# Performance work log

Measured on AMD Instinct MI355X. Metric: run time of the kernel, lower is better.

The kernel has to match this reference:

```python
import jax, jax.numpy as jnp
import numpy as np

B, H, L, D = 2, 16, 1024, 64
LMAX = 2048  # max_sequence_length: patterns built & normalized at LMAX, then sliced to L
PI = float(np.pi)


def _scale_pattern(freq):
    # pattern[h, t, d] = exp(i(t+ph)) + exp(i(2t+ph)) + exp(i(0.5t+ph)), ph = 2*pi*h/H
    # identical across d, so keep [H, L, 1] and broadcast over D
    phase = 2.0 * PI * jnp.arange(H, dtype=jnp.float32) / H          # [H]
    t = jnp.linspace(0.0, 2.0 * PI * freq, LMAX)                     # [LMAX]
    a1 = t[None, :] + phase[:, None]
    a2 = 2.0 * t[None, :] + phase[:, None]
    a3 = 0.5 * t[None, :] + phase[:, None]
    pr = jnp.cos(a1) + jnp.cos(a2) + jnp.cos(a3)                     # [H, LMAX]
    pi_ = jnp.sin(a1) + jnp.sin(a2) + jnp.sin(a3)
    norm = jnp.sqrt(jnp.sum(pr * pr + pi_ * pi_, axis=1, keepdims=True))  # over full LMAX
    pr, pi_ = pr / norm, pi_ / norm
    return pr[:, :L, None], pi_[:, :L, None]                          # [H, L, 1]


def _expert_total_pattern():
    # 8 experts x 3 aspects; pattern[t, d] = exp(i(f*t + 2*pi*d/D)), normalized per
    # column over LMAX (|exp|=1 -> norm sqrt(LMAX)). Elementwise complex multiply is
    # linear, so the expert stage equals x * sum(all patterns)/(sqrt(3)*sqrt(8)).
    freqs = np.array([[0.3 + 0.1 * i, 0.2 + 0.1 * i, 0.1 + 0.1 * i]
                      for i in range(8)], dtype=np.float32).reshape(-1)   # [24]
    t = jnp.linspace(0.0, 2.0 * PI, LMAX)                                 # [LMAX]
    phase_d = 2.0 * PI * jnp.arange(D, dtype=jnp.float32) / D             # [D]
    ang = jnp.asarray(freqs)[:, None, None] * t[None, :, None] + phase_d[None, None, :]  # [24, LMAX, D]
    col_norm = 1.0 / np.sqrt(float(LMAX))
    denom = np.sqrt(3.0) * np.sqrt(8.0)
    pr = jnp.sum(jnp.cos(ang), axis=0) * (col_norm / denom)               # [LMAX, D]
    pi_ = jnp.sum(jnp.sin(ang), axis=0) * (col_norm / denom)
    return pr[:L], pi_[:L]                                                # [L, D]


def _process_scale(Qr, Qi, Kr, Ki, Vr, Vi, pr, pi_):
    # complex elementwise pattern multiply
    Qpr = Qr * pr - Qi * pi_
    Qpi = Qr * pi_ + Qi * pr
    Kpr = Kr * pr - Ki * pi_
    Kpi = Kr * pi_ + Ki * pr
    # complex scores = Qp @ Kp^T (no conjugation, matching the torch code)
    sr = jnp.einsum('bhld,bhmd->bhlm', Qpr, Kpr) - jnp.einsum('bhld,bhmd->bhlm', Qpi, Kpi)
    si = jnp.einsum('bhld,bhmd->bhlm', Qpr, Kpi) + jnp.einsum('bhld,bhmd->bhlm', Qpi, Kpr)
    mag = jnp.sqrt(sr * sr + si * si) / np.sqrt(float(D))
    w = jax.nn.softmax(mag, axis=-1)
    return (jnp.einsum('bhlm,bhmd->bhld', w, Vr),
            jnp.einsum('bhlm,bhmd->bhld', w, Vi))


def reference(Q_real, Q_imag, K_real, K_imag, V_real, V_imag):
    scale_freqs = [1.0, 0.5, 0.25, 0.1]  # char, word, phrase, sentence
    acc_r = jnp.zeros_like(Q_real)
    acc_i = jnp.zeros_like(Q_real)
    for f in scale_freqs:
        pr, pi_ = _scale_pattern(f)
        o_r, o_i = _process_scale(Q_real, Q_imag, K_real, K_imag, V_real, V_imag, pr, pi_)
        acc_r = acc_r + o_r
        acc_i = acc_i + o_i
    inv = 1.0 / np.sqrt(float(len(scale_freqs)))
    acc_r = acc_r * inv
    acc_i = acc_i * inv
    # expert mixing (linear in x -> single fused complex elementwise multiply)
    epr, epi = _expert_total_pattern()  # [L, D], broadcast over B,H
    out_r = acc_r * epr - acc_i * epi
    out_i = acc_r * epi + acc_i * epr
    return jnp.stack([out_r, out_i], axis=0)  # [2, B, H, L, D] (real, imag)


def setup_inputs() -> dict:
    key = jax.random.key(0)
    ks = jax.random.split(key, 6)
    shape = (B, H, L, D)
    names = ['Q_real', 'Q_imag', 'K_real', 'K_imag', 'V_real', 'V_imag']
    return {n: jax.random.normal(k, shape, dtype=jnp.float32) for n, k in zip(names, ks)}
```

## Files before the change

### kernel.cpp

```cpp
#include <hip/hip_runtime.h>
#include <math.h>

typedef short bf16x8 __attribute__((ext_vector_type(8)));
typedef float f32x4 __attribute__((ext_vector_type(4)));

#define BDIM 256
#define ADIM 512
constexpr int B_ = 2, H_ = 16, L_ = 1024, D_ = 64, LMAX_ = 2048;
constexpr int BH_ = B_ * H_;
constexpr float PI_F = 3.14159265358979323846f;

constexpr int WS_SVP = 0;
constexpr int WS_KBR = 65536;
constexpr int WS_KBI = WS_KBR + 1048576;
constexpr int WS_VTR = WS_KBI + 1048576;
constexpr int WS_VTI = WS_VTR + 1048576;

__device__ __forceinline__ unsigned short f2b(float x) {
    union { float f; unsigned u; } v; v.f = x;
    return (unsigned short)((v.u + 0x8000u) >> 16);
}
__device__ __forceinline__ float b2f(unsigned short x) {
    union { unsigned u; float f; } v; v.u = ((unsigned)x) << 16;
    return v.f;
}
__device__ __forceinline__ unsigned pk2(float a, float b) {
    union { float f; unsigned u; } va, vb; va.f = a; vb.f = b;
    return ((va.u + 0x8000u) >> 16) | ((vb.u + 0x8000u) & 0xFFFF0000u);
}
__device__ __forceinline__ uint4 pack4(const float4& a, const float4& b) {
    return make_uint4(pk2(a.x, a.y), pk2(a.z, a.w), pk2(b.x, b.y), pk2(b.z, b.w));
}
__device__ __forceinline__ unsigned cvtpk(float lo, float hi) {
    unsigned r;
    asm("v_cvt_pk_bf16_f32 %0, %1, %2" : "=v"(r) : "v"(lo), "v"(hi));
    return r;
}
__device__ __forceinline__ float vsqrt(float x) {
    float r;
    asm("v_sqrt_f32 %0, %1" : "=v"(r) : "v"(x));
    return r;
}

#define MFMA(a, b, c) __builtin_amdgcn_mfma_f32_16x16x32_bf16((a), (b), (c), 0, 0, 0)

__device__ __forceinline__ float a_val(int s, int l, float4 invn) {
    const float fr = (s == 0) ? 1.0f : (s == 1) ? 0.5f : (s == 2) ? 0.25f : 0.1f;
    const float iv = (s == 0) ? invn.x : (s == 1) ? invn.y : (s == 2) ? invn.z : invn.w;
    float t = (2.0f * PI_F * fr / (float)(LMAX_ - 1)) * (float)l;
    float m2 = 3.0f + 2.0f * cosf(t) + 2.0f * cosf(0.5f * t) + 2.0f * cosf(1.5f * t);
    return sqrtf(fmaxf(m2, 0.0f)) * iv;
}

__global__ __launch_bounds__(BDIM)
void prep_kernel(const float* __restrict__ Kr, const float* __restrict__ Ki,
                 const float* __restrict__ Vr, const float* __restrict__ Vi,
                 float* __restrict__ ws) {
    const int tid = threadIdx.x;
    const int blk = blockIdx.x;
    unsigned short* KbR = (unsigned short*)(ws + WS_KBR);
    unsigned short* KbI = (unsigned short*)(ws + WS_KBI);
    unsigned short* VtR = (unsigned short*)(ws + WS_VTR);
    unsigned short* VtI = (unsigned short*)(ws + WS_VTI);

    if (blk < 256) {
        const int comp = blk >> 7;
        const float* src = comp ? Ki : Kr;
        unsigned short* dst = comp ? KbI : KbR;
        size_t b0 = (size_t)(blk & 127) * 16384;
#pragma unroll
        for (int i = 0; i < 4; ++i) {
            size_t e = b0 + (size_t)(i * 256 + tid) * 16;
            float4 x0 = *(const float4*)(src + e);
            float4 x1 = *(const float4*)(src + e + 4);
            float4 x2 = *(const float4*)(src + e + 8);
            float4 x3 = *(const float4*)(src + e + 12);
            *(uint4*)(dst + e) = pack4(x0, x1);
            *(uint4*)(dst + e + 8) = pack4(x2, x3);
        }
    } else {
        __shared__ unsigned short sT[64 * 70];
        __shared__ float sRed[4 * 64];
        const int vb = blk - 256;
        const int comp = vb & 1, mt = (vb >> 1) & 15, bh = vb >> 5;
        const int m0 = mt * 64;
        const float* src = (comp ? Vi : Vr) + (size_t)bh * 65536 + (size_t)m0 * 64;
        unsigned short* dstA = (comp ? VtI : VtR) + (size_t)bh * 65536;
#pragma unroll
        for (int i = 0; i < 4; ++i) {
            int e = i * 256 + tid;
            int m = e >> 4, d4 = (e & 15) * 4;
            float4 x = *(const float4*)(src + (size_t)m * 64 + d4);
            *(uint2*)&sT[m * 70 + d4] = make_uint2(pk2(x.x, x.y), pk2(x.z, x.w));
        }
        {
            int d = tid & 63, grp = tid >> 6;
            float s = 0.0f;
#pragma unroll
            for (int k = 0; k < 16; ++k) s += src[(size_t)(grp * 16 + k) * 64 + d];
            sRed[grp * 64 + d] = s;
        }
        __syncthreads();
        {
            int d = tid >> 2, ms = (tid & 3) * 16;
            unsigned short v[16];
#pragma unroll
            for (int k = 0; k < 16; ++k) v[k] = sT[(ms + k) * 70 + d];
            unsigned short* dst = dstA + (size_t)d * 1024 + m0 + ms;
            *(uint4*)dst = make_uint4((unsigned)v[0] | ((unsigned)v[1] << 16),
                                      (unsigned)v[2] | ((unsigned)v[3] << 16),
                                      (unsigned)v[4] | ((unsigned)v[5] << 16),
                                      (unsigned)v[6] | ((unsigned)v[7] << 16));
            *(uint4*)(dst + 8) = make_uint4((unsigned)v[8] | ((unsigned)v[9] << 16),
                                            (unsigned)v[10] | ((unsigned)v[11] << 16),
                                            (unsigned)v[12] | ((unsigned)v[13] << 16),
                                            (unsigned)v[14] | ((unsigned)v[15] << 16));
        }
        if (tid < 64)
            ws[WS_SVP + comp * 32768 + bh * 1024 + tid * 16 + mt] =
                sRed[tid] + sRed[64 + tid] + sRed[128 + tid] + sRed[192 + tid];
    }
}

__device__ __forceinline__ void stage64s(const unsigned short* g0, int stride,
                                         unsigned short* lds, int w, int lane) {
#pragma unroll
    for (int i = 0; i < 2; ++i) {
        int c = w * 2 + i;
        int lrow = c * 8 + (lane >> 3);
        int lg = (lane & 7) ^ (lrow & 7);
        const unsigned short* src = g0 + (size_t)lrow * stride + lg * 8;
        __builtin_amdgcn_global_load_lds(
            (const __attribute__((address_space(1))) void*)src,
            (__attribute__((address_space(3))) void*)(lds + c * 512), 16, 0, 0);
    }
}
__device__ __forceinline__ bf16x8 ldfrag(const unsigned short* b, int row, int g) {
    return *(const bf16x8*)&b[row * 64 + ((g ^ (row & 7)) << 3)];
}

constexpr int OFF_DEN = 0;
constexpr int OFF_K0  = 2048;
constexpr int OFF_K1  = OFF_K0 + 16384;
constexpr int OFF_V0  = OFF_K1 + 16384;
constexpr int OFF_V1  = OFF_V0 + 16384;
constexpr int OFF_E   = OFF_V1 + 16384;
constexpr int OFF_MG  = OFF_E + 16384;
constexpr int OFF_AMB = OFF_MG + 16384;
constexpr int SMEM_BYTES = OFF_AMB + 8256;

__global__ __launch_bounds__(ADIM, 2)
void attn_kernel_w(const float* __restrict__ Qr, const float* __restrict__ Qi,
                   const float* __restrict__ ws, float* __restrict__ out, float4 invn) {
    extern __shared__ char smem[];
    float* sDen = (float*)(smem + OFF_DEN);
    unsigned short* sK0 = (unsigned short*)(smem + OFF_K0);
    unsigned short* sK1 = (unsigned short*)(smem + OFF_K1);
    unsigned short* sV0 = (unsigned short*)(smem + OFF_V0);
    unsigned short* sV1 = (unsigned short*)(smem + OFF_V1);
    unsigned short* sE  = (unsigned short*)(smem + OFF_E);
    unsigned short* sMg = (unsigned short*)(smem + OFF_MG);
    unsigned short* sAmb = (unsigned short*)(smem + OFF_AMB);

    const int tid = threadIdx.x;
    const int lane = tid & 63;
    const int w = tid >> 6;
    const int lo16 = lane & 15;
    const int quad = lane >> 4;
    const int blk = blockIdx.x;
    const int bh = (blk & 7) * 4 + (blk >> 6);
    const int qt = (blk >> 3) & 7;
    const int l0 = qt * 128;
    const size_t base = (size_t)bh * (L_ * D_);

    const unsigned short* gKr = (const unsigned short*)(ws + WS_KBR) + (size_t)bh * 65536;
    const unsigned short* gKi = (const unsigned short*)(ws + WS_KBI) + (size_t)bh * 65536;
    const unsigned short* gVr = (const unsigned short*)(ws + WS_VTR) + (size_t)bh * 65536;
    const unsigned short* gVi = (const unsigned short*)(ws + WS_VTI) + (size_t)bh * 65536;

    if (w < 4) {
        stage64s(gKr, 64, sK0, w, lane);
        stage64s(gKi, 64, sK1, w, lane);
    } else {
        stage64s(gVr, 1024, sV0, w - 4, lane);
        stage64s(gVi, 1024, sV1, w - 4, lane);
    }

    for (int e = tid; e < 4096; e += ADIM) {
        int s = e >> 10, l = e & 1023;
        sAmb[s * 1032 + l] = f2b(a_val(s, l, invn) * 0.125f);
    }

    bf16x8 fQr0, fQr1, fQi0, fQi1, fnQi0, fnQi1;
    {
        const int ql = l0 + w * 16 + lo16;
        const float* qr = Qr + base + (size_t)ql * 64;
        const float* qi = Qi + base + (size_t)ql * 64;
        float4 a0 = *(const float4*)(qr + quad * 8);
        float4 a1 = *(const float4*)(qr + quad * 8 + 4);
        float4 b0 = *(const float4*)(qr + 32 + quad * 8);
        float4 b1 = *(const float4*)(qr + 32 + quad * 8 + 4);
        *(uint4*)&fQr0 = pack4(a0, a1);
        *(uint4*)&fQr1 = pack4(b0, b1);
        a0 = *(const float4*)(qi + quad * 8);
        a1 = *(const float4*)(qi + quad * 8 + 4);
        b0 = *(const float4*)(qi + 32 + quad * 8);
        b1 = *(const float4*)(qi + 32 + quad * 8 + 4);
        *(uint4*)&fQi0 = pack4(a0, a1);
        *(uint4*)&fQi1 = pack4(b0, b1);
        uint4 t0 = *(uint4*)&fQi0, t1 = *(uint4*)&fQi1;
        t0.x ^= 0x80008000u; t0.y ^= 0x80008000u; t0.z ^= 0x80008000u; t0.w ^= 0x80008000u;
        t1.x ^= 0x80008000u; t1.y ^= 0x80008000u; t1.z ^= 0x80008000u; t1.w ^= 0x80008000u;
        *(uint4*)&fnQi0 = t0; *(uint4*)&fnQi1 = t1;
    }

    __syncthreads();

    bf16x8 uf1a = (bf16x8){0, 0, 0, 0, 0, 0, 0, 0};
    uf1a[0] = (short)f2b(b2f(sAmb[quad * 1032 + (l0 + w * 16 + lo16)]) *
                         (1.0f / 128.0f));

    f32x4 accM1 = (f32x4){0.f, 0.f, 0.f, 0.f};
    f32x4 aOutR[4], aOutI[4];
#pragma unroll
    for (int dt = 0; dt < 4; ++dt) {
        aOutR[dt] = (f32x4){0.f, 0.f, 0.f, 0.f};
        aOutI[dt] = (f32x4){0.f, 0.f, 0.f, 0.f};
    }

#pragma unroll 1
    for (int mt = 0; mt < 16; ++mt) {
        const int m0 = mt * 64;
        const int cur = mt & 1;
        if (mt < 15) {
            if (w < 4) {
                stage64s(gKr + (size_t)(m0 + 64) * 64, 64, sK0 + (cur ^ 1) * 4096, w, lane);
                stage64s(gKi + (size_t)(m0 + 64) * 64, 64, sK1 + (cur ^ 1) * 4096, w, lane);
            } else {
                stage64s(gVr + m0 + 64, 1024, sV0 + (cur ^ 1) * 4096, w - 4, lane);
                stage64s(gVi + m0 + 64, 1024, sV1 + (cur ^ 1) * 4096, w - 4, lane);
            }
        }
        const unsigned short* cK0 = sK0 + cur * 4096;
        const unsigned short* cK1 = sK1 + cur * 4096;
        const unsigned short* cV0 = sV0 + cur * 4096;
        const unsigned short* cV1 = sV1 + cur * 4096;

#pragma unroll
        for (int ct = 0; ct < 4; ++ct) {
            const int mrow = ct * 16 + lo16;
            bf16x8 kr0 = ldfrag(cK0, mrow, quad), kr1 = ldfrag(cK0, mrow, quad + 4);
            bf16x8 ki0 = ldfrag(cK1, mrow, quad), ki1 = ldfrag(cK1, mrow, quad + 4);
            f32x4 aR = (f32x4){0.f, 0.f, 0.f, 0.f};
            f32x4 aI = (f32x4){0.f, 0.f, 0.f, 0.f};
            __builtin_amdgcn_s_setprio(1);
            aR = MFMA(kr0, fQr0, aR);  aR = MFMA(kr1, fQr1, aR);
            aR = MFMA(ki0, fnQi0, aR); aR = MFMA(ki1, fnQi1, aR);
            aI = MFMA(ki0, fQr0, aI);  aI = MFMA(ki1, fQr1, aI);
            aI = MFMA(kr0, fQi0, aI);  aI = MFMA(kr1, fQi1, aI);
            __builtin_amdgcn_s_setprio(0);
            float mg0 = vsqrt(fmaf(aR[0], aR[0], aI[0] * aI[0]));
            float mg1 = vsqrt(fmaf(aR[1], aR[1], aI[1] * aI[1]));
            float mg2 = vsqrt(fmaf(aR[2], aR[2], aI[2] * aI[2]));
            float mg3 = vsqrt(fmaf(aR[3], aR[3], aI[3] * aI[3]));
            bf16x8 bf1 = (bf16x8){0, 0, 0, 0, 0, 0, 0, 0};
            bf1[0] = (short)sAmb[quad * 1032 + m0 + ct * 16 + lo16];
            f32x4 z = (f32x4){0.f, 0.f, 0.f, 0.f};
            f32x4 a1 = MFMA(bf1, uf1a, z);
            float p0 = mg0 * a1[0], p1 = mg1 * a1[1];
            float p2 = mg2 * a1[2], p3 = mg3 * a1[3];
            int l = w * 16 + lo16;
            int gph = (ct * 2 + (quad >> 1)) ^ (l & 7);
            *(uint2*)&sE[l * 64 + gph * 8 + (quad & 1) * 4] =
                make_uint2(cvtpk(p0, p1), cvtpk(p2, p3));
            *(uint2*)&sMg[l * 64 + gph * 8 + (quad & 1) * 4] =
                make_uint2(cvtpk(mg0, mg1), cvtpk(mg2, mg3));
        }
        {
            bf16x8 mf0 = ldfrag(sMg, w * 16 + lo16, quad);
            bf16x8 mf1 = ldfrag(sMg, w * 16 + lo16, quad + 4);
            bf16x8 b0 = (bf16x8){0, 0, 0, 0, 0, 0, 0, 0};
            bf16x8 b1 = (bf16x8){0, 0, 0, 0, 0, 0, 0, 0};
            if (lo16 < 4) {
                b0 = *(const bf16x8*)&sAmb[lo16 * 1032 + m0 + quad * 8];
                b1 = *(const bf16x8*)&sAmb[lo16 * 1032 + m0 + 32 + quad * 8];
            }
            accM1 = MFMA(mf0, b0, accM1);
            accM1 = MFMA(mf1, b1, accM1);
        }
        {
            bf16x8 pa0 = ldfrag(sE, w * 16 + lo16, quad);
            bf16x8 pa1 = ldfrag(sE, w * 16 + lo16, quad + 4);
            __builtin_amdgcn_s_setprio(1);
#pragma unroll
            for (int dt = 0; dt < 4; ++dt) {
                int dr = dt * 16 + lo16;
                bf16x8 vr0 = ldfrag(cV0, dr, quad), vr1 = ldfrag(cV0, dr, quad + 4);
                bf16x8 vi0 = ldfrag(cV1, dr, quad), vi1 = ldfrag(cV1, dr, quad + 4);
                aOutR[dt] = MFMA(pa0, vr0, aOutR[dt]);
                aOutR[dt] = MFMA(pa1, vr1, aOutR[dt]);
                aOutI[dt] = MFMA(pa0, vi0, aOutI[dt]);
                aOutI[dt] = MFMA(pa1, vi1, aOutI[dt]);
            }
            __builtin_amdgcn_s_setprio(0);
        }
        asm volatile("s_waitcnt vmcnt(0)" ::: "memory");
        __builtin_amdgcn_s_barrier();
    }

    if (lo16 < 4) {
#pragma unroll
        for (int reg = 0; reg < 4; ++reg) {
            int r = w * 16 + quad * 4 + reg;
            float alv = b2f(sAmb[lo16 * 1032 + (l0 + r)]) * 8.0f;
            sDen[lo16 * 128 + r] = 1.0f / (1024.0f + alv * accM1[reg]);
        }
    }
    float cden[4];
#pragma unroll
    for (int reg = 0; reg < 4; ++reg) {
        int r = w * 16 + quad * 4 + reg;
        cden[reg] = sDen[r] + sDen[128 + r] + sDen[256 + r] + sDen[384 + r];
    }

    const float cE = rsqrtf(2048.0f) * rsqrtf(24.0f);
    float eRr[4], eRi[4];
#pragma unroll
    for (int reg = 0; reg < 4; ++reg) {
        int lrow = l0 + w * 16 + quad * 4 + reg;
        float tl = (2.0f * PI_F / (float)(LMAX_ - 1)) * (float)lrow;
        float s1, c1;
        __sincosf(0.1f * tl, &s1, &c1);
        const float W[10] = {1.f, 2.f, 3.f, 3.f, 3.f, 3.f, 3.f, 3.f, 2.f, 1.f};
        float cr = c1, ci = s1;
        float er = W[0] * cr, ei = W[0] * ci;
#pragma unroll
        for (int k = 1; k < 10; ++k) {
            float nr = cr * c1 - ci * s1;
            float ni = cr * s1 + ci * c1;
            cr = nr; ci = ni;
            er = fmaf(W[k], cr, er);
            ei = fmaf(W[k], ci, ei);
        }
        eRr[reg] = er * cE;
        eRi[reg] = ei * cE;
    }

    const size_t ooff = (size_t)BH_ * L_ * D_;
#pragma unroll
    for (int dt = 0; dt < 4; ++dt) {
        int d = dt * 16 + lo16;
        const float* svp = ws + WS_SVP + bh * 1024 + (size_t)d * 16;
        float4 r0 = *(const float4*)(svp);
        float4 r1 = *(const float4*)(svp + 4);
        float4 r2 = *(const float4*)(svp + 8);
        float4 r3 = *(const float4*)(svp + 12);
        float svr = (r0.x + r0.y + r0.z + r0.w) + (r1.x + r1.y + r1.z + r1.w) +
                    (r2.x + r2.y + r2.z + r2.w) + (r3.x + r3.y + r3.z + r3.w);
        const float* svq = svp + 32768;
        r0 = *(const float4*)(svq);
        r1 = *(const float4*)(svq + 4);
        r2 = *(const float4*)(svq + 8);
        r3 = *(const float4*)(svq + 12);
        float svi = (r0.x + r0.y + r0.z + r0.w) + (r1.x + r1.y + r1.z + r1.w) +
                    (r2.x + r2.y + r2.z + r2.w) + (r3.x + r3.y + r3.z + r3.w);
        float sp, cp;
        __sincosf((2.0f * PI_F / 64.0f) * (float)d, &sp, &cp);
#pragma unroll
        for (int reg = 0; reg < 4; ++reg) {
            int lrow = l0 + w * 16 + quad * 4 + reg;
            float numR = fmaf(cden[reg], svr, aOutR[dt][reg]) * 0.5f;
            float numI = fmaf(cden[reg], svi, aOutI[dt][reg]) * 0.5f;
            float epr = cp * eRr[reg] - sp * eRi[reg];
            float epi = sp * eRr[reg] + cp * eRi[reg];
            size_t o = base + (size_t)lrow * 64 + d;
            out[o] = numR * epr - numI * epi;
            out[o + ooff] = numR * epi + numI * epr;
        }
    }
}

__global__ __launch_bounds__(BDIM, 2)
void attn_kernel(const float* __restrict__ Qr, const float* __restrict__ Qi,
                 const float* __restrict__ ws, float* __restrict__ out, float4 invn) {
    __shared__ unsigned short sK0[2][4096], sK1[2][4096];
    __shared__ unsigned short sV0[4096], sV1[4096];
    __shared__ unsigned short sE[4096];
    __shared__ unsigned short sMg[4096];
    __shared__ unsigned short sAmb[4 * 1032];
    __shared__ float sDen[4 * 64];

    const int tid = threadIdx.x;
    const int lane = tid & 63;
    const int w = tid >> 6;
    const int lo16 = lane & 15;
    const int quad = lane >> 4;
    const int blk = blockIdx.x;
    const int bh = (blk & 7) * 4 + (blk >> 7);
    const int qt = (blk >> 3) & 15;
    const int l0 = qt * 64;
    const size_t base = (size_t)bh * (L_ * D_);

    const unsigned short* gKr = (const unsigned short*)(ws + WS_KBR) + (size_t)bh * 65536;
    const unsigned short* gKi = (const unsigned short*)(ws + WS_KBI) + (size_t)bh * 65536;
    const unsigned short* gVr = (const unsigned short*)(ws + WS_VTR) + (size_t)bh * 65536;
    const unsigned short* gVi = (const unsigned short*)(ws + WS_VTI) + (size_t)bh * 65536;

    stage64s(gKr, 64, sK0[0], w, lane);
    stage64s(gKi, 64, sK1[0], w, lane);

    for (int e = tid; e < 4096; e += BDIM) {
        int s = e >> 10, l = e & 1023;
        sAmb[s * 1032 + l] = f2b(a_val(s, l, invn) * 0.125f);
    }

    bf16x8 fQr0, fQr1, fQi0, fQi1, fnQi0, fnQi1;
    {
        const int ql = l0 + w * 16 + lo16;
        const float* qr = Qr + base + (size_t)ql * 64;
        const float* qi = Qi + base + (size_t)ql * 64;
        float4 a0 = *(const float4*)(qr + quad * 8);
        float4 a1 = *(const float4*)(qr + quad * 8 + 4);
        float4 b0 = *(const float4*)(qr + 32 + quad * 8);
        float4 b1 = *(const float4*)(qr + 32 + quad * 8 + 4);
        *(uint4*)&fQr0 = pack4(a0, a1);
        *(uint4*)&fQr1 = pack4(b0, b1);
        a0 = *(const float4*)(qi + quad * 8);
        a1 = *(const float4*)(qi + quad * 8 + 4);
        b0 = *(const float4*)(qi + 32 + quad * 8);
        b1 = *(const float4*)(qi + 32 + quad * 8 + 4);
        *(uint4*)&fQi0 = pack4(a0, a1);
        *(uint4*)&fQi1 = pack4(b0, b1);
        uint4 t0 = *(uint4*)&fQi0, t1 = *(uint4*)&fQi1;
        t0.x ^= 0x80008000u; t0.y ^= 0x80008000u; t0.z ^= 0x80008000u; t0.w ^= 0x80008000u;
        t1.x ^= 0x80008000u; t1.y ^= 0x80008000u; t1.z ^= 0x80008000u; t1.w ^= 0x80008000u;
        *(uint4*)&fnQi0 = t0; *(uint4*)&fnQi1 = t1;
    }

    __syncthreads();

    bf16x8 uf1a = (bf16x8){0, 0, 0, 0, 0, 0, 0, 0};
    uf1a[0] = (short)f2b(b2f(sAmb[quad * 1032 + (l0 + w * 16 + lo16)]) *
                         (1.0f / 128.0f));

    f32x4 accM1 = (f32x4){0.f, 0.f, 0.f, 0.f};
    f32x4 aOutR[4], aOutI[4];
#pragma unroll
    for (int dt = 0; dt < 4; ++dt) {
        aOutR[dt] = (f32x4){0.f, 0.f, 0.f, 0.f};
        aOutI[dt] = (f32x4){0.f, 0.f, 0.f, 0.f};
    }

#pragma unroll 1
    for (int mt = 0; mt < 16; ++mt) {
        const int m0 = mt * 64;
        const int cur = mt & 1;
        stage64s(gVr + m0, 1024, sV0, w, lane);
        stage64s(gVi + m0, 1024, sV1, w, lane);
        if (mt < 15) {
            stage64s(gKr + (size_t)(m0 + 64) * 64, 64, sK0[cur ^ 1], w, lane);
            stage64s(gKi + (size_t)(m0 + 64) * 64, 64, sK1[cur ^ 1], w, lane);
        }
        const unsigned short* cK0 = sK0[cur];
        const unsigned short* cK1 = sK1[cur];

#pragma unroll
        for (int ct = 0; ct < 4; ++ct) {
            const int mrow = ct * 16 + lo16;
            bf16x8 kr0 = ldfrag(cK0, mrow, quad), kr1 = ldfrag(cK0, mrow, quad + 4);
            bf16x8 ki0 = ldfrag(cK1, mrow, quad), ki1 = ldfrag(cK1, mrow, quad + 4);
            f32x4 aR = (f32x4){0.f, 0.f, 0.f, 0.f};
            f32x4 aI = (f32x4){0.f, 0.f, 0.f, 0.f};
            __builtin_amdgcn_s_setprio(1);
            aR = MFMA(kr0, fQr0, aR);  aR = MFMA(kr1, fQr1, aR);
            aR = MFMA(ki0, fnQi0, aR); aR = MFMA(ki1, fnQi1, aR);
            aI = MFMA(ki0, fQr0, aI);  aI = MFMA(ki1, fQr1, aI);
            aI = MFMA(kr0, fQi0, aI);  aI = MFMA(kr1, fQi1, aI);
            __builtin_amdgcn_s_setprio(0);
            float mg0 = vsqrt(fmaf(aR[0], aR[0], aI[0] * aI[0]));
            float mg1 = vsqrt(fmaf(aR[1], aR[1], aI[1] * aI[1]));
            float mg2 = vsqrt(fmaf(aR[2], aR[2], aI[2] * aI[2]));
            float mg3 = vsqrt(fmaf(aR[3], aR[3], aI[3] * aI[3]));
            bf16x8 bf1 = (bf16x8){0, 0, 0, 0, 0, 0, 0, 0};
            bf1[0] = (short)sAmb[quad * 1032 + m0 + ct * 16 + lo16];
            f32x4 z = (f32x4){0.f, 0.f, 0.f, 0.f};
            f32x4 a1 = MFMA(bf1, uf1a, z);
            float p0 = mg0 * a1[0], p1 = mg1 * a1[1];
            float p2 = mg2 * a1[2], p3 = mg3 * a1[3];
            int l = w * 16 + lo16;
            int gph = (ct * 2 + (quad >> 1)) ^ (l & 7);
            *(uint2*)&sE[l * 64 + gph * 8 + (quad & 1) * 4] =
                make_uint2(cvtpk(p0, p1), cvtpk(p2, p3));
            *(uint2*)&sMg[l * 64 + gph * 8 + (quad & 1) * 4] =
                make_uint2(cvtpk(mg0, mg1), cvtpk(mg2, mg3));
        }
        {
            bf16x8 mf0 = ldfrag(sMg, w * 16 + lo16, quad);
            bf16x8 mf1 = ldfrag(sMg, w * 16 + lo16, quad + 4);
            bf16x8 b0 = (bf16x8){0, 0, 0, 0, 0, 0, 0, 0};
            bf16x8 b1 = (bf16x8){0, 0, 0, 0, 0, 0, 0, 0};
            if (lo16 < 4) {
                b0 = *(const bf16x8*)&sAmb[lo16 * 1032 + m0 + quad * 8];
                b1 = *(const bf16x8*)&sAmb[lo16 * 1032 + m0 + 32 + quad * 8];
            }
            accM1 = MFMA(mf0, b0, accM1);
            accM1 = MFMA(mf1, b1, accM1);
        }
        if (mt < 15) {
            asm volatile("s_waitcnt vmcnt(4)" ::: "memory");
        } else {
            asm volatile("s_waitcnt vmcnt(0)" ::: "memory");
        }
        __builtin_amdgcn_s_barrier();
        {
            bf16x8 pa0 = ldfrag(sE, w * 16 + lo16, quad);
            bf16x8 pa1 = ldfrag(sE, w * 16 + lo16, quad + 4);
            __builtin_amdgcn_s_setprio(1);
#pragma unroll
            for (int dt = 0; dt < 4; ++dt) {
                int dr = dt * 16 + lo16;
                bf16x8 vr0 = ldfrag(sV0, dr, quad), vr1 = ldfrag(sV0, dr, quad + 4);
                bf16x8 vi0 = ldfrag(sV1, dr, quad), vi1 = ldfrag(sV1, dr, quad + 4);
                aOutR[dt] = MFMA(pa0, vr0, aOutR[dt]);
                aOutR[dt] = MFMA(pa1, vr1, aOutR[dt]);
                aOutI[dt] = MFMA(pa0, vi0, aOutI[dt]);
                aOutI[dt] = MFMA(pa1, vi1, aOutI[dt]);
            }
            __builtin_amdgcn_s_setprio(0);
        }
        asm volatile("s_waitcnt vmcnt(0)" ::: "memory");
        __builtin_amdgcn_s_barrier();
    }

    if (lo16 < 4) {
#pragma unroll
        for (int reg = 0; reg < 4; ++reg) {
            int r = w * 16 + quad * 4 + reg;
            float alv = b2f(sAmb[lo16 * 1032 + (l0 + r)]) * 8.0f;
            sDen[lo16 * 64 + r] = 1.0f / (1024.0f + alv * accM1[reg]);
        }
    }
    float cden[4];
#pragma unroll
    for (int reg = 0; reg < 4; ++reg) {
        int r = w * 16 + quad * 4 + reg;
        cden[reg] = sDen[r] + sDen[64 + r] + sDen[128 + r] + sDen[192 + r];
    }

    const float cE = rsqrtf(2048.0f) * rsqrtf(24.0f);
    float eRr[4], eRi[4];
#pragma unroll
    for (int reg = 0; reg < 4; ++reg) {
        int lrow = l0 + w * 16 + quad * 4 + reg;
        float tl = (2.0f * PI_F / (float)(LMAX_ - 1)) * (float)lrow;
        float s1, c1;
        __sincosf(0.1f * tl, &s1, &c1);
        const float W[10] = {1.f, 2.f, 3.f, 3.f, 3.f, 3.f, 3.f, 3.f, 2.f, 1.f};
        float cr = c1, ci = s1;
        float er = W[0] * cr, ei = W[0] * ci;
#pragma unroll
        for (int k = 1; k < 10; ++k) {
            float nr = cr * c1 - ci * s1;
            float ni = cr * s1 + ci * c1;
            cr = nr; ci = ni;
            er = fmaf(W[k], cr, er);
            ei = fmaf(W[k], ci, ei);
        }
        eRr[reg] = er * cE;
        eRi[reg] = ei * cE;
    }

    const size_t ooff = (size_t)BH_ * L_ * D_;
#pragma unroll
    for (int dt = 0; dt < 4; ++dt) {
        int d = dt * 16 + lo16;
        const float* svp = ws + WS_SVP + bh * 1024 + (size_t)d * 16;
        float4 r0 = *(const float4*)(svp);
        float4 r1 = *(const float4*)(svp + 4);
        float4 r2 = *(const float4*)(svp + 8);
        float4 r3 = *(const float4*)(svp + 12);
        float svr = (r0.x + r0.y + r0.z + r0.w) + (r1.x + r1.y + r1.z + r1.w) +
                    (r2.x + r2.y + r2.z + r2.w) + (r3.x + r3.y + r3.z + r3.w);
        const float* svq = svp + 32768;
        r0 = *(const float4*)(svq);
        r1 = *(const float4*)(svq + 4);
        r2 = *(const float4*)(svq + 8);
        r3 = *(const float4*)(svq + 12);
        float svi = (r0.x + r0.y + r0.z + r0.w) + (r1.x + r1.y + r1.z + r1.w) +
                    (r2.x + r2.y + r2.z + r2.w) + (r3.x + r3.y + r3.z + r3.w);
        float sp, cp;
        __sincosf((2.0f * PI_F / 64.0f) * (float)d, &sp, &cp);
#pragma unroll
        for (int reg = 0; reg < 4; ++reg) {
            int lrow = l0 + w * 16 + quad * 4 + reg;
            float numR = fmaf(cden[reg], svr, aOutR[dt][reg]) * 0.5f;
            float numI = fmaf(cden[reg], svi, aOutI[dt][reg]) * 0.5f;
            float epr = cp * eRr[reg] - sp * eRi[reg];
            float epi = sp * eRr[reg] + cp * eRi[reg];
            size_t o = base + (size_t)lrow * 64 + d;
            out[o] = numR * epr - numI * epi;
            out[o + ooff] = numR * epi + numI * epr;
        }
    }
}

extern "C" void kernel_launch(void* const* d_in, const int* in_sizes, int n_in,
                              void* d_out, int out_size, void* d_ws, size_t ws_size,
                              hipStream_t stream) {
    const float* Qr = (const float*)d_in[0];
    const float* Qi = (const float*)d_in[1];
    const float* Kr = (const float*)d_in[2];
    const float* Ki = (const float*)d_in[3];
    const float* Vr = (const float*)d_in[4];
    const float* Vi = (const float*)d_in[5];
    float* ws = (float*)d_ws;
    float* out = (float*)d_out;

    const double fr[4] = {1.0, 0.5, 0.25, 0.1};
    float inv[4];
    for (int s = 0; s < 4; ++s) {
        double a = 2.0 * 3.14159265358979323846 * fr[s] / (double)(LMAX_ - 1);
        double S = 3.0 * LMAX_;
        const double mul[3] = {1.0, 0.5, 1.5};
        for (int k = 0; k < 3; ++k) {
            double x = a * mul[k];
            S += 2.0 * (cos(x * 1023.5) * sin(x * 1024.0) / sin(x * 0.5));
        }
        inv[s] = (float)(1.0 / sqrt(S));
    }
    float4 invn = make_float4(inv[0], inv[1], inv[2], inv[3]);

    prep_kernel<<<1280, BDIM, 0, stream>>>(Kr, Ki, Vr, Vi, ws);

    static int wideOK = -1;
    if (wideOK < 0) {
        hipError_t e = hipFuncSetAttribute(
            reinterpret_cast<const void*>(attn_kernel_w),
            hipFuncAttributeMaxDynamicSharedMemorySize, SMEM_BYTES);
        wideOK = (e == hipSuccess) ? 1 : 0;
    }
    if (wideOK)
        attn_kernel_w<<<256, ADIM, SMEM_BYTES, stream>>>(Qr, Qi, ws, out, invn);
    else
        attn_kernel<<<512, BDIM, 0, stream>>>(Qr, Qi, ws, out, invn);
}
```

Measured before the change: 138.8 us.

## Software-pipeline QK^T of tile m with PV of tile m-1 in wide attention kernel

Restructures the 512-thread attention main loop so the score/weight computation for the current K tile is interleaved with the P·V MFMAs for the previous tile. It triple-buffers V and double-buffers the weight tile in LDS, adding a prologue and epilogue, which removes the intra-iteration dependency between writing sE and reading it. The QK^T accumulation is also split into independent MFMA chains to shorten dependency latency. The cost is more LDS per block, which may reduce occupancy, plus larger code and more register pressure from the interleaving.

```diff
diff --git a/kernel.cpp b/kernel.cpp
--- a/kernel.cpp
+++ b/kernel.cpp
@@ -143,9 +143,9 @@
 constexpr int OFF_K0  = 2048;
 constexpr int OFF_K1  = OFF_K0 + 16384;
 constexpr int OFF_V0  = OFF_K1 + 16384;
-constexpr int OFF_V1  = OFF_V0 + 16384;
-constexpr int OFF_E   = OFF_V1 + 16384;
-constexpr int OFF_MG  = OFF_E + 16384;
+constexpr int OFF_V1  = OFF_V0 + 24576;
+constexpr int OFF_E   = OFF_V1 + 24576;
+constexpr int OFF_MG  = OFF_E + 32768;
 constexpr int OFF_AMB = OFF_MG + 16384;
 constexpr int SMEM_BYTES = OFF_AMB + 8256;
 
@@ -228,23 +228,290 @@
         aOutI[dt] = (f32x4){0.f, 0.f, 0.f, 0.f};
     }
 
+    const int lrow_w = w * 16 + lo16;
+
+#define QKT_PHASE(cK0_, cK1_, eDst_, m0_, ct_)                                     \
+    {                                                                              \
+        const int mrow = (ct_) * 16 + lo16;                                        \
+        bf16x8 kr0 = ldfrag((cK0_), mrow, quad), kr1 = ldfrag((cK0_), mrow, quad + 4); \
+        bf16x8 ki0 = ldfrag((cK1_), mrow, quad), ki1 = ldfrag((cK1_), mrow, quad + 4); \
+        f32x4 z = (f32x4){0.f, 0.f, 0.f, 0.f};                                     \
+        __builtin_amdgcn_s_setprio(1);                                             \
+        f32x4 aRa = MFMA(kr0, fQr0, z);  aRa = MFMA(ki0, fnQi0, aRa);              \
+        f32x4 aRb = MFMA(kr1, fQr1, z);  aRb = MFMA(ki1, fnQi1, aRb);              \
+        f32x4 aIa = MFMA(ki0, fQr0, z);  aIa = MFMA(kr0, fQi0, aIa);               \
+        f32x4 aIb = MFMA(ki1, fQr1, z);  aIb = MFMA(kr1, fQi1, aIb);               \
+        __builtin_amdgcn_s_setprio(0);                                             \
+        f32x4 aR = aRa + aRb, aI = aIa + aIb;                                      \
+        float mg0 = vsqrt(fmaf(aR[0], aR[0], aI[0] * aI[0]));                      \
+        float mg1 = vsqrt(fmaf(aR[1], aR[1], aI[1] * aI[1]));                      \
+        float mg2 = vsqrt(fmaf(aR[2], aR[2], aI[2] * aI[2]));                      \
+        float mg3 = vsqrt(fmaf(aR[3], aR[3], aI[3] * aI[3]));                      \
+        bf16x8 bf1 = (bf16x8){0, 0, 0, 0, 0, 0, 0, 0};                             \
+        bf1[0] = (short)sAmb[quad * 1032 + (m0_) + (ct_) * 16 + lo16];             \
+        f32x4 a1 = MFMA(bf1, uf1a, z);                                             \
+        float p0 = mg0 * a1[0], p1 = mg1 * a1[1];                                  \
+        float p2 = mg2 * a1[2], p3 = mg3 * a1[3];                                  \
+        int gph = ((ct_) * 2 + (quad >> 1)) ^ (lrow_w & 7);                        \
+        *(uint2*)&(eDst_)[lrow_w * 64 + gph * 8 + (quad & 1) * 4] =                \
+            make_uint2(cvtpk(p0, p1), cvtpk(p2, p3));                              \
+        *(uint2*)&sMg[lrow_w * 64 + gph * 8 + (quad & 1) * 4] =                    \
+            make_uint2(cvtpk(mg0, mg1), cvtpk(mg2, mg3));                          \
+    }
+
+#define M1_STEP(m0_)                                                               \
+    {                                                                              \
+        bf16x8 mf0 = ldfrag(sMg, lrow_w, quad);                                    \
+        bf16x8 mf1 = ldfrag(sMg, lrow_w, quad + 4);                                \
+        bf16x8 b0 = (bf16x8){0, 0, 0, 0, 0, 0, 0, 0};                              \
+        bf16x8 b1 = (bf16x8){0, 0, 0, 0, 0, 0, 0, 0};                              \
+        if (lo16 < 4) {                                                            \
+            b0 = *(const bf16x8*)&sAmb[lo16 * 1032 + (m0_) + quad * 8];            \
+            b1 = *(const bf16x8*)&sAmb[lo16 * 1032 + (m0_) + 32 + quad * 8];       \
+        }                                                                          \
+        accM1 = MFMA(mf0, b0, accM1);                                              \
+        accM1 = MFMA(mf1, b1, accM1);                                              \
+    }
+
+#define PV_PHASE(pV0_, pV1_, pa0_, pa1_, dt_)                                      \
+    {                                                                              \
+        int dr = (dt_) * 16 + lo16;                                                \
+        bf16x8 vr0 = ldfrag((pV0_), dr, quad), vr1 = ldfrag((pV0_), dr, quad + 4); \
+        bf16x8 vi0 = ldfrag((pV1_), dr, quad), vi1 = ldfrag((pV1_), dr, quad + 4); \
+        __builtin_amdgcn_s_setprio(1);                                             \
+        aOutR[dt_] = MFMA((pa0_), vr0, aOutR[dt_]);                                \
+        aOutR[dt_] = MFMA((pa1_), vr1, aOutR[dt_]);                                \
+        aOutI[dt_] = MFMA((pa0_), vi0, aOutI[dt_]);                                \
+        aOutI[dt_] = MFMA((pa1_), vi1, aOutI[dt_]);                                \
+        __builtin_amdgcn_s_setprio(0);                                             \
+    }
+
+    {
+        if (w < 4) {
+            stage64s(gKr + (size_t)64 * 64, 64, sK0 + 4096, w, lane);
+            stage64s(gKi + (size_t)64 * 64, 64, sK1 + 4096, w, lane);
+        } else {
+            stage64s(gVr + 64, 1024, sV0 + 4096, w - 4, lane);
+            stage64s(gVi + 64, 1024, sV1 + 4096, w - 4, lane);
+        }
+        QKT_PHASE(sK0, sK1, sE, 0, 0)
+        QKT_PHASE(sK0, sK1, sE, 0, 1)
+        QKT_PHASE(sK0, sK1, sE, 0, 2)
+        QKT_PHASE(sK0, sK1, sE, 0, 3)
+        M1_STEP(0)
+        asm volatile("s_waitcnt vmcnt(0)" ::: "memory");
+        __builtin_amdgcn_s_barrier();
+    }
+
+#pragma unroll 1
+    for (int mt = 1; mt < 16; ++mt) {
+        const int m0 = mt * 64;
+        const int cur = mt & 1;
+        const int vprev = (mt - 1) % 3;
+        if (mt < 15) {
+            const int vnext = (mt + 1) % 3;
+            if (w < 4) {
+                stage64s(gKr + (size_t)(m0 + 64) * 64, 64, sK0 + (cur ^ 1) * 4096, w, lane);
+                stage64s(gKi + (size_t)(m0 + 64) * 64, 64, sK1 + (cur ^ 1) * 4096, w, lane);
+            } else {
+                stage64s(gVr + m0 + 64, 1024, sV0 + vnext * 4096, w - 4, lane);
+                stage64s(gVi + m0 + 64, 1024, sV1 + vnext * 4096, w - 4, lane);
+            }
+        }
+        const unsigned short* cK0 = sK0 + cur * 4096;
+        const unsigned short* cK1 = sK1 + cur * 4096;
+        const unsigned short* pV0 = sV0 + vprev * 4096;
+        const unsigned short* pV1 = sV1 + vprev * 4096;
+        unsigned short* eCur = sE + cur * 8192;
+        const unsigned short* ePrev = sE + (cur ^ 1) * 8192;
+
+        bf16x8 pa0 = ldfrag(ePrev, lrow_w, quad);
+        bf16x8 pa1 = ldfrag(ePrev, lrow_w, quad + 4);
+
+        QKT_PHASE(cK0, cK1, eCur, m0, 0)
+        PV_PHASE(pV0, pV1, pa0, pa1, 0)
+        QKT_PHASE(cK0, cK1, eCur, m0, 1)
+        PV_PHASE(pV0, pV1, pa0, pa1, 1)
+        QKT_PHASE(cK0, cK1, eCur, m0, 2)
+        PV_PHASE(pV0, pV1, pa0, pa1, 2)
+        QKT_PHASE(cK0, cK1, eCur, m0, 3)
+        PV_PHASE(pV0, pV1, pa0, pa1, 3)
+        M1_STEP(m0)
+
+        asm volatile("s_waitcnt vmcnt(0)" ::: "memory");
+        __builtin_amdgcn_s_barrier();
+    }
+
+    {
+        const unsigned short* pV0 = sV0;
+        const unsigned short* pV1 = sV1;
+        const unsigned short* ePrev = sE + 8192;
+        bf16x8 pa0 = ldfrag(ePrev, lrow_w, quad);
+        bf16x8 pa1 = ldfrag(ePrev, lrow_w, quad + 4);
+        PV_PHASE(pV0, pV1, pa0, pa1, 0)
+        PV_PHASE(pV0, pV1, pa0, pa1, 1)
+        PV_PHASE(pV0, pV1, pa0, pa1, 2)
+        PV_PHASE(pV0, pV1, pa0, pa1, 3)
+    }
+
+    if (lo16 < 4) {
+#pragma unroll
+        for (int reg = 0; reg < 4; ++reg) {
+            int r = w * 16 + quad * 4 + reg;
+            float alv = b2f(sAmb[lo16 * 1032 + (l0 + r)]) * 8.0f;
+            sDen[lo16 * 128 + r] = 1.0f / (1024.0f + alv * accM1[reg]);
+        }
+    }
+    float cden[4];
+#pragma unroll
+    for (int reg = 0; reg < 4; ++reg) {
+        int r = w * 16 + quad * 4 + reg;
+        cden[reg] = sDen[r] + sDen[128 + r] + sDen[256 + r] + sDen[384 + r];
+    }
+
+    const float cE = rsqrtf(2048.0f) * rsqrtf(24.0f);
+    float eRr[4], eRi[4];
+#pragma unroll
+    for (int reg = 0; reg < 4; ++reg) {
+        int lrow = l0 + w * 16 + quad * 4 + reg;
+        float tl = (2.0f * PI_F / (float)(LMAX_ - 1)) * (float)lrow;
+        float s1, c1;
+        __sincosf(0.1f * tl, &s1, &c1);
+        const float W[10] = {1.f, 2.f, 3.f, 3.f, 3.f, 3.f, 3.f, 3.f, 2.f, 1.f};
+        float cr = c1, ci = s1;
+        float er = W[0] * cr, ei = W[0] * ci;
+#pragma unroll
+        for (int k = 1; k < 10; ++k) {
+            float nr = cr * c1 - ci * s1;
+            float ni = cr * s1 + ci * c1;
+            cr = nr; ci = ni;
+            er = fmaf(W[k], cr, er);
+            ei = fmaf(W[k], ci, ei);
+        }
+        eRr[reg] = er * cE;
+        eRi[reg] = ei * cE;
+    }
+
+    const size_t ooff = (size_t)BH_ * L_ * D_;
+#pragma unroll
+    for (int dt = 0; dt < 4; ++dt) {
+        int d = dt * 16 + lo16;
+        const float* svp = ws + WS_SVP + bh * 1024 + (size_t)d * 16;
+        float4 r0 = *(const float4*)(svp);
+        float4 r1 = *(const float4*)(svp + 4);
+        float4 r2 = *(const float4*)(svp + 8);
+        float4 r3 = *(const float4*)(svp + 12);
+        float svr = (r0.x + r0.y + r0.z + r0.w) + (r1.x + r1.y + r1.z + r1.w) +
+                    (r2.x + r2.y + r2.z + r2.w) + (r3.x + r3.y + r3.z + r3.w);
+        const float* svq = svp + 32768;
+        r0 = *(const float4*)(svq);
+        r1 = *(const float4*)(svq + 4);
+        r2 = *(const float4*)(svq + 8);
+        r3 = *(const float4*)(svq + 12);
+        float svi = (r0.x + r0.y + r0.z + r0.w) + (r1.x + r1.y + r1.z + r1.w) +
+                    (r2.x + r2.y + r2.z + r2.w) + (r3.x + r3.y + r3.z + r3.w);
+        float sp, cp;
+        __sincosf((2.0f * PI_F / 64.0f) * (float)d, &sp, &cp);
+#pragma unroll
+        for (int reg = 0; reg < 4; ++reg) {
+            int lrow = l0 + w * 16 + quad * 4 + reg;
+            float numR = fmaf(cden[reg], svr, aOutR[dt][reg]) * 0.5f;
+            float numI = fmaf(cden[reg], svi, aOutI[dt][reg]) * 0.5f;
+            float epr = cp * eRr[reg] - sp * eRi[reg];
+            float epi = sp * eRr[reg] + cp * eRi[reg];
+            size_t o = base + (size_t)lrow * 64 + d;
+            out[o] = numR * epr - numI * epi;
+            out[o + ooff] = numR * epi + numI * epr;
+        }
+    }
+#undef QKT_PHASE
+#undef M1_STEP
+#undef PV_PHASE
+}
+
+__global__ __launch_bounds__(BDIM, 2)
+void attn_kernel(const float* __restrict__ Qr, const float* __restrict__ Qi,
+                 const float* __restrict__ ws, float* __restrict__ out, float4 invn) {
+    __shared__ unsigned short sK0[2][4096], sK1[2][4096];
+    __shared__ unsigned short sV0[4096], sV1[4096];
+    __shared__ unsigned short sE[4096];
+    __shared__ unsigned short sMg[4096];
+    __shared__ unsigned short sAmb[4 * 1032];
+    __shared__ float sDen[4 * 64];
+
+    const int tid = threadIdx.x;
+    const int lane = tid & 63;
+    const int w = tid >> 6;
+    const int lo16 = lane & 15;
+    const int quad = lane >> 4;
+    const int blk = blockIdx.x;
+    const int bh = (blk & 7) * 4 + (blk >> 7);
+    const int qt = (blk >> 3) & 15;
+    const int l0 = qt * 64;
+    const size_t base = (size_t)bh * (L_ * D_);
+
+    const unsigned short* gKr = (const unsigned short*)(ws + WS_KBR) + (size_t)bh * 65536;
+    const unsigned short* gKi = (const unsigned short*)(ws + WS_KBI) + (size_t)bh * 65536;
+    const unsigned short* gVr = (const unsigned short*)(ws + WS_VTR) + (size_t)bh * 65536;
+    const unsigned short* gVi = (const unsigned short*)(ws + WS_VTI) + (size_t)bh * 65536;
+
+    stage64s(gKr, 64, sK0[0], w, lane);
+    stage64s(gKi, 64, sK1[0], w, lane);
+
+    for (int e = tid; e < 4096; e += BDIM) {
+        int s = e >> 10, l = e & 1023;
+        sAmb[s * 1032 + l] = f2b(a_val(s, l, invn) * 0.125f);
+    }
+
+    bf16x8 fQr0, fQr1, fQi0, fQi1, fnQi0, fnQi1;
+    {
+        const int ql = l0 + w * 16 + lo16;
+        const float* qr = Qr + base + (size_t)ql * 64;
+        const float* qi = Qi + base + (size_t)ql * 64;
+        float4 a0 = *(const float4*)(qr + quad * 8);
+        float4 a1 = *(const float4*)(qr + quad * 8 + 4);
+        float4 b0 = *(const float4*)(qr + 32 + quad * 8);
+        float4 b1 = *(const float4*)(qr + 32 + quad * 8 + 4);
+        *(uint4*)&fQr0 = pack4(a0, a1);
+        *(uint4*)&fQr1 = pack4(b0, b1);
+        a0 = *(const float4*)(qi + quad * 8);
+        a1 = *(const float4*)(qi + quad * 8 + 4);
+        b0 = *(const float4*)(qi + 32 + quad * 8);
+        b1 = *(const float4*)(qi + 32 + quad * 8 + 4);
+        *(uint4*)&fQi0 = pack4(a0, a1);
+        *(uint4*)&fQi1 = pack4(b0, b1);
+        uint4 t0 = *(uint4*)&fQi0, t1 = *(uint4*)&fQi1;
+        t0.x ^= 0x80008000u; t0.y ^= 0x80008000u; t0.z ^= 0x80008000u; t0.w ^= 0x80008000u;
+        t1.x ^= 0x80008000u; t1.y ^= 0x80008000u; t1.z ^= 0x80008000u; t1.w ^= 0x80008000u;
+        *(uint4*)&fnQi0 = t0; *(uint4*)&fnQi1 = t1;
+    }
+
+    __syncthreads();
+
+    bf16x8 uf1a = (bf16x8){0, 0, 0, 0, 0, 0, 0, 0};
+    uf1a[0] = (short)f2b(b2f(sAmb[quad * 1032 + (l0 + w * 16 + lo16)]) *
+                         (1.0f / 128.0f));
+
+    f32x4 accM1 = (f32x4){0.f, 0.f, 0.f, 0.f};
+    f32x4 aOutR[4], aOutI[4];
+#pragma unroll
+    for (int dt = 0; dt < 4; ++dt) {
+        aOutR[dt] = (f32x4){0.f, 0.f, 0.f, 0.f};
+        aOutI[dt] = (f32x4){0.f, 0.f, 0.f, 0.f};
+    }
+
 #pragma unroll 1
     for (int mt = 0; mt < 16; ++mt) {
         const int m0 = mt * 64;
         const int cur = mt & 1;
+        stage64s(gVr + m0, 1024, sV0, w, lane);
+        stage64s(gVi + m0, 1024, sV1, w, lane);
         if (mt < 15) {
-            if (w < 4) {
-                stage64s(gKr + (size_t)(m0 + 64) * 64, 64, sK0 + (cur ^ 1) * 4096, w, lane);
-                stage64s(gKi + (size_t)(m0 + 64) * 64, 64, sK1 + (cur ^ 1) * 4096, w, lane);
-            } else {
-                stage64s(gVr + m0 + 64, 1024, sV0 + (cur ^ 1) * 4096, w - 4, lane);
-                stage64s(gVi + m0 + 64, 1024, sV1 + (cur ^ 1) * 4096, w - 4, lane);
-            }
-        }
-        const unsigned short* cK0 = sK0 + cur * 4096;
-        const unsigned short* cK1 = sK1 + cur * 4096;
-        const unsigned short* cV0 = sV0 + cur * 4096;
-        const unsigned short* cV1 = sV1 + cur * 4096;
+            stage64s(gKr + (size_t)(m0 + 64) * 64, 64, sK0[cur ^ 1], w, lane);
+            stage64s(gKi + (size_t)(m0 + 64) * 64, 64, sK1[cur ^ 1], w, lane);
+        }
+        const unsigned short* cK0 = sK0[cur];
+        const unsigned short* cK1 = sK1[cur];
 
 #pragma unroll
         for (int ct = 0; ct < 4; ++ct) {
@@ -288,6 +555,12 @@
             accM1 = MFMA(mf0, b0, accM1);
             accM1 = MFMA(mf1, b1, accM1);
         }
+        if (mt < 15) {
+            asm volatile("s_waitcnt vmcnt(4)" ::: "memory");
+        } else {
+            asm volatile("s_waitcnt vmcnt(0)" ::: "memory");
+        }
+        __builtin_amdgcn_s_barrier();
         {
             bf16x8 pa0 = ldfrag(sE, w * 16 + lo16, quad);
             bf16x8 pa1 = ldfrag(sE, w * 16 + lo16, quad + 4);
@@ -295,8 +568,8 @@
 #pragma unroll
             for (int dt = 0; dt < 4; ++dt) {
                 int dr = dt * 16 + lo16;
-                bf16x8 vr0 = ldfrag(cV0, dr, quad), vr1 = ldfrag(cV0, dr, quad + 4);
-                bf16x8 vi0 = ldfrag(cV1, dr, quad), vi1 = ldfrag(cV1, dr, quad + 4);
+                bf16x8 vr0 = ldfrag(sV0, dr, quad), vr1 = ldfrag(sV0, dr, quad + 4);
+                bf16x8 vi0 = ldfrag(sV1, dr, quad), vi1 = ldfrag(sV1, dr, quad + 4);
                 aOutR[dt] = MFMA(pa0, vr0, aOutR[dt]);
                 aOutR[dt] = MFMA(pa1, vr1, aOutR[dt]);
                 aOutI[dt] = MFMA(pa0, vi0, aOutI[dt]);
@@ -313,14 +586,14 @@
         for (int reg = 0; reg < 4; ++reg) {
             int r = w * 16 + quad * 4 + reg;
             float alv = b2f(sAmb[lo16 * 1032 + (l0 + r)]) * 8.0f;
-            sDen[lo16 * 128 + r] = 1.0f / (1024.0f + alv * accM1[reg]);
+            sDen[lo16 * 64 + r] = 1.0f / (1024.0f + alv * accM1[reg]);
         }
     }
     float cden[4];
 #pragma unroll
     for (int reg = 0; reg < 4; ++reg) {
         int r = w * 16 + quad * 4 + reg;
-        cden[reg] = sDen[r] + sDen[128 + r] + sDen[256 + r] + sDen[384 + r];
+        cden[reg] = sDen[r] + sDen[64 + r] + sDen[128 + r] + sDen[192 + r];
     }
 
     const float cE = rsqrtf(2048.0f) * rsqrtf(24.0f);
@@ -380,230 +653,6 @@
     }
 }
 
-__global__ __launch_bounds__(BDIM, 2)
-void attn_kernel(const float* __restrict__ Qr, const float* __restrict__ Qi,
-                 const float* __restrict__ ws, float* __restrict__ out, float4 invn) {
-    __shared__ unsigned short sK0[2][4096], sK1[2][4096];
-    __shared__ unsigned short sV0[4096], sV1[4096];
-    __shared__ unsigned short sE[4096];
-    __shared__ unsigned short sMg[4096];
-    __shared__ unsigned short sAmb[4 * 1032];
-    __shared__ float sDen[4 * 64];
-
-    const int tid = threadIdx.x;
-    const int lane = tid & 63;
-    const int w = tid >> 6;
-    const int lo16 = lane & 15;
-    const int quad = lane >> 4;
-    const int blk = blockIdx.x;
-    const int bh = (blk & 7) * 4 + (blk >> 7);
-    const int qt = (blk >> 3) & 15;
-    const int l0 = qt * 64;
-    const size_t base = (size_t)bh * (L_ * D_);
-
-    const unsigned short* gKr = (const unsigned short*)(ws + WS_KBR) + (size_t)bh * 65536;
-    const unsigned short* gKi = (const unsigned short*)(ws + WS_KBI) + (size_t)bh * 65536;
-    const unsigned short* gVr = (const unsigned short*)(ws + WS_VTR) + (size_t)bh * 65536;
-    const unsigned short* gVi = (const unsigned short*)(ws + WS_VTI) + (size_t)bh * 65536;
-
-    stage64s(gKr, 64, sK0[0], w, lane);
-    stage64s(gKi, 64, sK1[0], w, lane);
-
-    for (int e = tid; e < 4096; e += BDIM) {
-        int s = e >> 10, l = e & 1023;
-        sAmb[s * 1032 + l] = f2b(a_val(s, l, invn) * 0.125f);
-    }
-
-    bf16x8 fQr0, fQr1, fQi0, fQi1, fnQi0, fnQi1;
-    {
-        const int ql = l0 + w * 16 + lo16;
-        const float* qr = Qr + base + (size_t)ql * 64;
-        const float* qi = Qi + base + (size_t)ql * 64;
-        float4 a0 = *(const float4*)(qr + quad * 8);
-        float4 a1 = *(const float4*)(qr + quad * 8 + 4);
-        float4 b0 = *(const float4*)(qr + 32 + quad * 8);
-        float4 b1 = *(const float4*)(qr + 32 + quad * 8 + 4);
-        *(uint4*)&fQr0 = pack4(a0, a1);
-        *(uint4*)&fQr1 = pack4(b0, b1);
-        a0 = *(const float4*)(qi + quad * 8);
-        a1 = *(const float4*)(qi + quad * 8 + 4);
-        b0 = *(const float4*)(qi + 32 + quad * 8);
-        b1 = *(const float4*)(qi + 32 + quad * 8 + 4);
-        *(uint4*)&fQi0 = pack4(a0, a1);
-        *(uint4*)&fQi1 = pack4(b0, b1);
-        uint4 t0 = *(uint4*)&fQi0, t1 = *(uint4*)&fQi1;
-        t0.x ^= 0x80008000u; t0.y ^= 0x80008000u; t0.z ^= 0x80008000u; t0.w ^= 0x80008000u;
-        t1.x ^= 0x80008000u; t1.y ^= 0x80008000u; t1.z ^= 0x80008000u; t1.w ^= 0x80008000u;
-        *(uint4*)&fnQi0 = t0; *(uint4*)&fnQi1 = t1;
-    }
-
-    __syncthreads();
-
-    bf16x8 uf1a = (bf16x8){0, 0, 0, 0, 0, 0, 0, 0};
-    uf1a[0] = (short)f2b(b2f(sAmb[quad * 1032 + (l0 + w * 16 + lo16)]) *
-                         (1.0f / 128.0f));
-
-    f32x4 accM1 = (f32x4){0.f, 0.f, 0.f, 0.f};
-    f32x4 aOutR[4], aOutI[4];
-#pragma unroll
-    for (int dt = 0; dt < 4; ++dt) {
-        aOutR[dt] = (f32x4){0.f, 0.f, 0.f, 0.f};
-        aOutI[dt] = (f32x4){0.f, 0.f, 0.f, 0.f};
-    }
-
-#pragma unroll 1
-    for (int mt = 0; mt < 16; ++mt) {
-        const int m0 = mt * 64;
-        const int cur = mt & 1;
-        stage64s(gVr + m0, 1024, sV0, w, lane);
-        stage64s(gVi + m0, 1024, sV1, w, lane);
-        if (mt < 15) {
-            stage64s(gKr + (size_t)(m0 + 64) * 64, 64, sK0[cur ^ 1], w, lane);
-            stage64s(gKi + (size_t)(m0 + 64) * 64, 64, sK1[cur ^ 1], w, lane);
-        }
-        const unsigned short* cK0 = sK0[cur];
-        const unsigned short* cK1 = sK1[cur];
-
-#pragma unroll
-        for (int ct = 0; ct < 4; ++ct) {
-            const int mrow = ct * 16 + lo16;
-            bf16x8 kr0 = ldfrag(cK0, mrow, quad), kr1 = ldfrag(cK0, mrow, quad + 4);
-            bf16x8 ki0 = ldfrag(cK1, mrow, quad), ki1 = ldfrag(cK1, mrow, quad + 4);
-            f32x4 aR = (f32x4){0.f, 0.f, 0.f, 0.f};
-            f32x4 aI = (f32x4){0.f, 0.f, 0.f, 0.f};
-            __builtin_amdgcn_s_setprio(1);
-            aR = MFMA(kr0, fQr0, aR);  aR = MFMA(kr1, fQr1, aR);
-            aR = MFMA(ki0, fnQi0, aR); aR = MFMA(ki1, fnQi1, aR);
-            aI = MFMA(ki0, fQr0, aI);  aI = MFMA(ki1, fQr1, aI);
-            aI = MFMA(kr0, fQi0, aI);  aI = MFMA(kr1, fQi1, aI);
-            __builtin_amdgcn_s_setprio(0);
-            float mg0 = vsqrt(fmaf(aR[0], aR[0], aI[0] * aI[0]));
-            float mg1 = vsqrt(fmaf(aR[1], aR[1], aI[1] * aI[1]));
-            float mg2 = vsqrt(fmaf(aR[2], aR[2], aI[2] * aI[2]));
-            float mg3 = vsqrt(fmaf(aR[3], aR[3], aI[3] * aI[3]));
-            bf16x8 bf1 = (bf16x8){0, 0, 0, 0, 0, 0, 0, 0};
-            bf1[0] = (short)sAmb[quad * 1032 + m0 + ct * 16 + lo16];
-            f32x4 z = (f32x4){0.f, 0.f, 0.f, 0.f};
-            f32x4 a1 = MFMA(bf1, uf1a, z);
-            float p0 = mg0 * a1[0], p1 = mg1 * a1[1];
-            float p2 = mg2 * a1[2], p3 = mg3 * a1[3];
-            int l = w * 16 + lo16;
-            int gph = (ct * 2 + (quad >> 1)) ^ (l & 7);
-            *(uint2*)&sE[l * 64 + gph * 8 + (quad & 1) * 4] =
-                make_uint2(cvtpk(p0, p1), cvtpk(p2, p3));
-            *(uint2*)&sMg[l * 64 + gph * 8 + (quad & 1) * 4] =
-                make_uint2(cvtpk(mg0, mg1), cvtpk(mg2, mg3));
-        }
-        {
-            bf16x8 mf0 = ldfrag(sMg, w * 16 + lo16, quad);
-            bf16x8 mf1 = ldfrag(sMg, w * 16 + lo16, quad + 4);
-            bf16x8 b0 = (bf16x8){0, 0, 0, 0, 0, 0, 0, 0};
-            bf16x8 b1 = (bf16x8){0, 0, 0, 0, 0, 0, 0, 0};
-            if (lo16 < 4) {
-                b0 = *(const bf16x8*)&sAmb[lo16 * 1032 + m0 + quad * 8];
-                b1 = *(const bf16x8*)&sAmb[lo16 * 1032 + m0 + 32 + quad * 8];
-            }
-            accM1 = MFMA(mf0, b0, accM1);
-            accM1 = MFMA(mf1, b1, accM1);
-        }
-        if (mt < 15) {
-            asm volatile("s_waitcnt vmcnt(4)" ::: "memory");
-        } else {
-            asm volatile("s_waitcnt vmcnt(0)" ::: "memory");
-        }
-        __builtin_amdgcn_s_barrier();
-        {
-            bf16x8 pa0 = ldfrag(sE, w * 16 + lo16, quad);
-            bf16x8 pa1 = ldfrag(sE, w * 16 + lo16, quad + 4);
-            __builtin_amdgcn_s_setprio(1);
-#pragma unroll
-            for (int dt = 0; dt < 4; ++dt) {
-                int dr = dt * 16 + lo16;
-                bf16x8 vr0 = ldfrag(sV0, dr, quad), vr1 = ldfrag(sV0, dr, quad + 4);
-                bf16x8 vi0 = ldfrag(sV1, dr, quad), vi1 = ldfrag(sV1, dr, quad + 4);
-                aOutR[dt] = MFMA(pa0, vr0, aOutR[dt]);
-                aOutR[dt] = MFMA(pa1, vr1, aOutR[dt]);
-                aOutI[dt] = MFMA(pa0, vi0, aOutI[dt]);
-                aOutI[dt] = MFMA(pa1, vi1, aOutI[dt]);
-            }
-            __builtin_amdgcn_s_setprio(0);
-        }
-        asm volatile("s_waitcnt vmcnt(0)" ::: "memory");
-        __builtin_amdgcn_s_barrier();
-    }
-
-    if (lo16 < 4) {
-#pragma unroll
-        for (int reg = 0; reg < 4; ++reg) {
-            int r = w * 16 + quad * 4 + reg;
-            float alv = b2f(sAmb[lo16 * 1032 + (l0 + r)]) * 8.0f;
-            sDen[lo16 * 64 + r] = 1.0f / (1024.0f + alv * accM1[reg]);
-        }
-    }
-    float cden[4];
-#pragma unroll
-    for (int reg = 0; reg < 4; ++reg) {
-        int r = w * 16 + quad * 4 + reg;
-        cden[reg] = sDen[r] + sDen[64 + r] + sDen[128 + r] + sDen[192 + r];
-    }
-
-    const float cE = rsqrtf(2048.0f) * rsqrtf(24.0f);
-    float eRr[4], eRi[4];
-#pragma unroll
-    for (int reg = 0; reg < 4; ++reg) {
-        int lrow = l0 + w * 16 + quad * 4 + reg;
-        float tl = (2.0f * PI_F / (float)(LMAX_ - 1)) * (float)lrow;
-        float s1, c1;
-        __sincosf(0.1f * tl, &s1, &c1);
-        const float W[10] = {1.f, 2.f, 3.f, 3.f, 3.f, 3.f, 3.f, 3.f, 2.f, 1.f};
-        float cr = c1, ci = s1;
-        float er = W[0] * cr, ei = W[0] * ci;
-#pragma unroll
-        for (int k = 1; k < 10; ++k) {
-            float nr = cr * c1 - ci * s1;
-            float ni = cr * s1 + ci * c1;
-            cr = nr; ci = ni;
-            er = fmaf(W[k], cr, er);
-            ei = fmaf(W[k], ci, ei);
-        }
-        eRr[reg] = er * cE;
-        eRi[reg] = ei * cE;
-    }
-
-    const size_t ooff = (size_t)BH_ * L_ * D_;
-#pragma unroll
-    for (int dt = 0; dt < 4; ++dt) {
-        int d = dt * 16 + lo16;
-        const float* svp = ws + WS_SVP + bh * 1024 + (size_t)d * 16;
-        float4 r0 = *(const float4*)(svp);
-        float4 r1 = *(const float4*)(svp + 4);
-        float4 r2 = *(const float4*)(svp + 8);
-        float4 r3 = *(const float4*)(svp + 12);
-        float svr = (r0.x + r0.y + r0.z + r0.w) + (r1.x + r1.y + r1.z + r1.w) +
-                    (r2.x + r2.y + r2.z + r2.w) + (r3.x + r3.y + r3.z + r3.w);
-        const float* svq = svp + 32768;
-        r0 = *(const float4*)(svq);
-        r1 = *(const float4*)(svq + 4);
-        r2 = *(const float4*)(svq + 8);
-        r3 = *(const float4*)(svq + 12);
-        float svi = (r0.x + r0.y + r0.z + r0.w) + (r1.x + r1.y + r1.z + r1.w) +
-                    (r2.x + r2.y + r2.z + r2.w) + (r3.x + r3.y + r3.z + r3.w);
-        float sp, cp;
-        __sincosf((2.0f * PI_F / 64.0f) * (float)d, &sp, &cp);
-#pragma unroll
-        for (int reg = 0; reg < 4; ++reg) {
-            int lrow = l0 + w * 16 + quad * 4 + reg;
-            float numR = fmaf(cden[reg], svr, aOutR[dt][reg]) * 0.5f;
-            float numI = fmaf(cden[reg], svi, aOutI[dt][reg]) * 0.5f;
-            float epr = cp * eRr[reg] - sp * eRi[reg];
-            float epi = sp * eRr[reg] + cp * eRi[reg];
-            size_t o = base + (size_t)lrow * 64 + d;
-            out[o] = numR * epr - numI * epi;
-            out[o + ooff] = numR * epi + numI * epr;
-        }
-    }
-}
-
 extern "C" void kernel_launch(void* const* d_in, const int* in_sizes, int n_in,
                               void* d_out, int out_size, void* d_ws, size_t ws_size,
                               hipStream_t stream) {
```

Result: no change. 139.2 us (+0.3%).
